# Performance work log

Measured on AMD Instinct MI355X. Metric: run time of the kernel, lower is better.

Reference implementation:

```python
import jax, jax.numpy as jnp
import numpy as np

NUM_BINS = 4
SCALE = 5.0
EPS = 1e-12

def hswish(x):
    return x * jnp.clip(x + 3.0, 0.0, 6.0) / 6.0

def l2norm(x, axis):
    n = jnp.sqrt(jnp.sum(x * x, axis=axis, keepdims=True))
    return x / jnp.maximum(n, EPS)

def setup_inputs() -> dict:
    key = jax.random.key(0)
    k0, k1, k2, k3, k4 = jax.random.split(key, 5)
    B, C, T, H, W = 8, 256, 32, 28, 28
    hidden, embd = 512, 32
    x = jax.random.normal(k0, (B, C, T, H, W), dtype=jnp.float32)
    W1 = jax.random.normal(k1, (hidden, C), dtype=jnp.float32) * (1.0 / np.sqrt(C))
    b1 = jax.random.normal(k2, (hidden,), dtype=jnp.float32) * 0.01
    W2 = jax.random.normal(k3, (embd, hidden), dtype=jnp.float32) * (1.0 / np.sqrt(hidden))
    b2 = jax.random.normal(k4, (embd,), dtype=jnp.float32) * 0.01
    return {"x": x, "W1": W1, "b1": b1, "W2": W2, "b2": b2}

def reference(x, W1, b1, W2, b2):
    B, C, T, H, W = x.shape
    # encoder: global spatial avg-pool -> 1x1x1 conv -> HSwish -> 1x1x1 conv
    pooled = jnp.mean(x, axis=(3, 4))                      # (B,C,T)
    h = hswish(jnp.einsum('hc,bct->bht', W1, pooled) + b1[None, :, None])
    embds = jnp.einsum('eh,bht->bet', W2, h) + b2[None, :, None]   # (B,E,T)
    norm_embd = l2norm(embds, axis=1)

    # --- grouping (no-grad in original) ---
    ns = jnp.sum(norm_embd[:, :, 1:] * norm_embd[:, :, :-1], axis=1)    # (B,T-1)
    # k-th smallest neighbour similarity = threshold
    smallest = -jax.lax.top_k(-ns, NUM_BINS - 1)[0]                      # ascending smallest k
    threshold = smallest[:, -1]
    edges = (ns > threshold[:, None]).astype(jnp.int32)                  # (B,T-1)
    interval_ends = jnp.concatenate(
        [jnp.zeros((B, 1), dtype=jnp.int32), 1 - edges], axis=1)        # (B,T)
    groups = jnp.cumsum(interval_ends, axis=1)                           # (B,T)
    group_ids = jnp.arange(NUM_BINS, dtype=groups.dtype)
    group_mask = (groups[:, :, None] == group_ids[None, None, :]).astype(jnp.float32)  # (B,T,K)
    group_sizes = jnp.sum(group_mask, axis=1, keepdims=True)             # (B,1,K)
    centers_sum = jnp.einsum('bet,btk->bek', norm_embd, group_mask)      # (B,E,K)
    norm_centers = l2norm(centers_sum / group_sizes, axis=1)             # (B,E,K)
    norm_centers = jax.lax.stop_gradient(norm_centers)

    similarities = jnp.einsum('bet,bek->btk', norm_embd, norm_centers)   # (B,T,K)
    weights = jax.nn.softmax(SCALE * similarities, axis=2)               # (B,T,K)
    sum_weights = jnp.sum(weights, axis=1, keepdims=True)                # (B,1,K)
    scales = jnp.where(sum_weights > 0.0, 1.0 / sum_weights, jnp.ones_like(sum_weights))
    scales = jax.lax.stop_gradient(scales)
    norm_weights = scales * weights                                      # (B,T,K)

    # weighted temporal pooling: avoids (B,C,T,K,H,W) blowup
    out = jnp.einsum('bcthw,btk->bckhw', x, norm_weights)                # (B,C,K,H,W)
    return out
```

## Files before the change

### kernel.cpp

```cpp
#include <hip/hip_runtime.h>
#include <math.h>

#define BATCH 8
#define CCH   256
#define TT    32
#define HWSZ  784
#define HID   512
#define EMB   32
#define KBINS 4
#define SCALEF 5.0f
#define EPSN  1e-12f

__global__ __launch_bounds__(512) void poolfc_kernel(
        const float* __restrict__ x,
        const float* __restrict__ W1, const float* __restrict__ b1,
        const float* __restrict__ W2, const float* __restrict__ b2,
        float* __restrict__ embds) {
    __shared__ float pc[CCH];
    __shared__ float hcol[HID];

    const int b    = blockIdx.x >> 5;
    const int t    = blockIdx.x & 31;
    const int tid  = threadIdx.x;
    const int wave = tid >> 6;
    const int lane = tid & 63;

    const float* xbt = x + (size_t)(b * CCH) * (TT * HWSZ) + (size_t)t * HWSZ;
#pragma unroll
    for (int i = 0; i < 16; ++i) {
        const int c0 = (i << 4) + wave;
        const int c1 = c0 + 8;
        const float4* xp0 = (const float4*)(xbt + (size_t)c0 * (TT * HWSZ));
        const float4* xp1 = (const float4*)(xbt + (size_t)c1 * (TT * HWSZ));
        float4 a0 = xp0[lane];
        float4 a1 = xp0[lane + 64];
        float4 a2 = xp0[lane + 128];
        float4 d0 = xp1[lane];
        float4 d1 = xp1[lane + 64];
        float4 d2 = xp1[lane + 128];
        float s0 = a0.x + a0.y + a0.z + a0.w
                 + a1.x + a1.y + a1.z + a1.w
                 + a2.x + a2.y + a2.z + a2.w;
        float s1 = d0.x + d0.y + d0.z + d0.w
                 + d1.x + d1.y + d1.z + d1.w
                 + d2.x + d2.y + d2.z + d2.w;
        if (lane < 4) {
            float4 a3 = xp0[lane + 192];
            float4 d3 = xp1[lane + 192];
            s0 += a3.x + a3.y + a3.z + a3.w;
            s1 += d3.x + d3.y + d3.z + d3.w;
        }
#pragma unroll
        for (int off = 32; off > 0; off >>= 1) {
            s0 += __shfl_down(s0, off);
            s1 += __shfl_down(s1, off);
        }
        if (lane == 0) {
            pc[c0] = s0 * (1.0f / 784.0f);
            pc[c1] = s1 * (1.0f / 784.0f);
        }
    }
    __syncthreads();

    {
        const float4* w = (const float4*)(W1 + (size_t)tid * CCH);
        const float4* p4 = (const float4*)pc;
        float acc = 0.f;
#pragma unroll 8
        for (int j = 0; j < CCH / 4; ++j) {
            float4 wv = w[j];
            float4 pv = p4[j];
            acc += wv.x * pv.x + wv.y * pv.y + wv.z * pv.z + wv.w * pv.w;
        }
        acc += b1[tid];
        float r = fminf(fmaxf(acc + 3.0f, 0.0f), 6.0f);
        hcol[tid] = acc * r * (1.0f / 6.0f);
    }
    __syncthreads();

    {
        const int e = tid >> 4;
        const int l = tid & 15;
        const float* w = W2 + (size_t)e * HID;
        float acc = 0.f;
#pragma unroll
        for (int j = 0; j < HID / 16; j++) acc += w[l + 16 * j] * hcol[l + 16 * j];
        acc += __shfl_down(acc, 8);
        acc += __shfl_down(acc, 4);
        acc += __shfl_down(acc, 2);
        acc += __shfl_down(acc, 1);
        if (l == 0) embds[((size_t)b * EMB + e) * TT + t] = acc + b2[e];
    }
}

__global__ void group_kernel(const float* __restrict__ embds, float* __restrict__ nw) {
    __shared__ float se[EMB][TT + 1];
    __shared__ float ns[TT];
    __shared__ float colinv[TT];
    __shared__ float thr_sh;
    __shared__ float cs[EMB][KBINS];
    __shared__ float wts[TT][KBINS];
    __shared__ float gsize[KBINS];
    __shared__ float kfac[KBINS];
    __shared__ int   gid[TT];

    const int b   = blockIdx.x;
    const int tid = threadIdx.x;

    for (int i = tid; i < EMB * TT; i += 256)
        se[i >> 5][i & 31] = embds[(size_t)b * EMB * TT + i];
    __syncthreads();

    if (tid < TT) {
        float s = 0.f;
        for (int e = 0; e < EMB; e++) { float v = se[e][tid]; s += v * v; }
        colinv[tid] = 1.0f / fmaxf(sqrtf(s), EPSN);
    }
    __syncthreads();
    for (int i = tid; i < EMB * TT; i += 256) {
        int e = i >> 5, t = i & 31;
        se[e][t] *= colinv[t];
    }
    __syncthreads();

    if (tid < TT - 1) {
        float s = 0.f;
        for (int e = 0; e < EMB; e++) s += se[e][tid] * se[e][tid + 1];
        ns[tid] = s;
    }
    __syncthreads();

    if (tid < TT - 1) {
        float v = ns[tid];
        int pos = 0;
        for (int j = 0; j < TT - 1; j++) {
            float u = ns[j];
            pos += (u < v) || (u == v && j < tid);
        }
        if (pos == KBINS - 2) thr_sh = v;
    }
    __syncthreads();

    if (tid < TT) {
        float thr = thr_sh;
        int g = 0;
        for (int s = 1; s <= tid; s++) g += !(ns[s - 1] > thr);
        gid[tid] = g;
    }
    __syncthreads();
    if (tid < KBINS) {
        float c = 0.f;
        for (int t = 0; t < TT; t++) c += (gid[t] == tid);
        gsize[tid] = c;
    }
    __syncthreads();

    if (tid < EMB * KBINS) {
        int e = tid >> 2, k = tid & 3;
        float s = 0.f;
        for (int t = 0; t < TT; t++) if (gid[t] == k) s += se[e][t];
        cs[e][k] = s / gsize[k];
    }
    __syncthreads();
    if (tid < KBINS) {
        float s = 0.f;
        for (int e = 0; e < EMB; e++) { float v = cs[e][tid]; s += v * v; }
        kfac[tid] = 1.0f / fmaxf(sqrtf(s), EPSN);
    }
    __syncthreads();
    if (tid < EMB * KBINS) {
        int e = tid >> 2, k = tid & 3;
        cs[e][k] *= kfac[k];
    }
    __syncthreads();

    if (tid < TT * KBINS) {
        int t = tid >> 2, k = tid & 3;
        float s = 0.f;
        for (int e = 0; e < EMB; e++) s += se[e][t] * cs[e][k];
        wts[t][k] = s * SCALEF;
    }
    __syncthreads();
    if (tid < TT) {
        float m = wts[tid][0];
        for (int k = 1; k < KBINS; k++) m = fmaxf(m, wts[tid][k]);
        float ex[KBINS]; float sum = 0.f;
        for (int k = 0; k < KBINS; k++) { ex[k] = expf(wts[tid][k] - m); sum += ex[k]; }
        float inv = 1.0f / sum;
        for (int k = 0; k < KBINS; k++) wts[tid][k] = ex[k] * inv;
    }
    __syncthreads();
    if (tid < KBINS) {
        float s = 0.f;
        for (int t = 0; t < TT; t++) s += wts[t][tid];
        kfac[tid] = (s > 0.f) ? (1.0f / s) : 1.0f;
    }
    __syncthreads();
    if (tid < TT * KBINS) {
        int t = tid >> 2, k = tid & 3;
        nw[((size_t)b * TT + t) * KBINS + k] = wts[t][k] * kfac[k];
    }
}

__global__ __launch_bounds__(128) void out_kernel(
        const float* __restrict__ x, const float* __restrict__ nw,
        float* __restrict__ out) {
    __shared__ float w[TT * KBINS];
    const int b = blockIdx.x / 392;
    const unsigned idx = (blockIdx.x % 392) * 128 + threadIdx.x;
    w[threadIdx.x] = nw[(size_t)b * TT * KBINS + threadIdx.x];
    __syncthreads();
    const unsigned c = idx / 196;
    const unsigned f = idx % 196;
    const float4* xp = (const float4*)(x + ((size_t)(b * CCH + c) * TT) * HWSZ);
    float4 acc[KBINS];
#pragma unroll
    for (int k = 0; k < KBINS; k++) { acc[k].x = 0.f; acc[k].y = 0.f; acc[k].z = 0.f; acc[k].w = 0.f; }
#pragma unroll 8
    for (int t = 0; t < TT; t++) {
        float4 v = xp[t * 196 + f];
#pragma unroll
        for (int k = 0; k < KBINS; k++) {
            float wk = w[t * KBINS + k];
            acc[k].x += v.x * wk;
            acc[k].y += v.y * wk;
            acc[k].z += v.z * wk;
            acc[k].w += v.w * wk;
        }
    }
    float4* op = (float4*)(out + ((size_t)(b * CCH + c) * KBINS) * HWSZ);
#pragma unroll
    for (int k = 0; k < KBINS; k++) op[k * 196 + f] = acc[k];
}

extern "C" void kernel_launch(void* const* d_in, const int* in_sizes, int n_in,
                              void* d_out, int out_size, void* d_ws, size_t ws_size,
                              hipStream_t stream) {
    const float* x  = (const float*)d_in[0];
    const float* W1 = (const float*)d_in[1];
    const float* b1 = (const float*)d_in[2];
    const float* W2 = (const float*)d_in[3];
    const float* b2 = (const float*)d_in[4];
    float* out = (float*)d_out;

    float* ws    = (float*)d_ws;
    float* embds = ws;
    float* nw    = embds + BATCH * EMB * TT;

    poolfc_kernel<<<BATCH * TT, 512, 0, stream>>>(x, W1, b1, W2, b2, embds);
    group_kernel<<<BATCH, 256, 0, stream>>>(embds, nw);
    out_kernel<<<BATCH * 392, 128, 0, stream>>>(x, nw, out);
}
```

Baseline: 346.1 us.

## Fuse grouping into weighted-pooling kernel, recomputing weights per block

Merges the per-batch grouping kernel into the output pooling kernel. Each of the 1568 blocks recomputes the normalized bin weights for its batch in shared memory and then does the temporal weighted sum over 256 threads, with the weights read as one float4 per timestep. This removes one kernel launch and the round trip of the weights through global memory. The cost is that the serial grouping logic (top-k, cumsum, softmax, many barriers) now runs redundantly in every block before any x loads are issued.

```diff
diff --git a/kernel.cpp b/kernel.cpp
--- a/kernel.cpp
+++ b/kernel.cpp
@@ -93,7 +93,9 @@
     }
 }
 
-__global__ void group_kernel(const float* __restrict__ embds, float* __restrict__ nw) {
+__global__ __launch_bounds__(256) void outg_kernel(
+        const float* __restrict__ x, const float* __restrict__ embds,
+        float* __restrict__ out) {
     __shared__ float se[EMB][TT + 1];
     __shared__ float ns[TT];
     __shared__ float colinv[TT];
@@ -103,8 +105,9 @@
     __shared__ float gsize[KBINS];
     __shared__ float kfac[KBINS];
     __shared__ int   gid[TT];
-
-    const int b   = blockIdx.x;
+    __shared__ float wl[TT * KBINS];
+
+    const int b   = blockIdx.x / 196;
     const int tid = threadIdx.x;
 
     for (int i = tid; i < EMB * TT; i += 256)
@@ -198,39 +201,33 @@
     __syncthreads();
     if (tid < TT * KBINS) {
         int t = tid >> 2, k = tid & 3;
-        nw[((size_t)b * TT + t) * KBINS + k] = wts[t][k] * kfac[k];
-    }
-}
-
-__global__ __launch_bounds__(128) void out_kernel(
-        const float* __restrict__ x, const float* __restrict__ nw,
-        float* __restrict__ out) {
-    __shared__ float w[TT * KBINS];
-    const int b = blockIdx.x / 392;
-    const unsigned idx = (blockIdx.x % 392) * 128 + threadIdx.x;
-    w[threadIdx.x] = nw[(size_t)b * TT * KBINS + threadIdx.x];
-    __syncthreads();
+        wl[tid] = wts[t][k] * kfac[k];
+    }
+    __syncthreads();
+
+    const unsigned idx = (blockIdx.x % 196) * 256 + tid;
     const unsigned c = idx / 196;
     const unsigned f = idx % 196;
     const float4* xp = (const float4*)(x + ((size_t)(b * CCH + c) * TT) * HWSZ);
-    float4 acc[KBINS];
-#pragma unroll
-    for (int k = 0; k < KBINS; k++) { acc[k].x = 0.f; acc[k].y = 0.f; acc[k].z = 0.f; acc[k].w = 0.f; }
+    const float4* wp = (const float4*)wl;
+    float4 a0 = {0.f, 0.f, 0.f, 0.f};
+    float4 a1 = {0.f, 0.f, 0.f, 0.f};
+    float4 a2 = {0.f, 0.f, 0.f, 0.f};
+    float4 a3 = {0.f, 0.f, 0.f, 0.f};
 #pragma unroll 8
-    for (int t = 0; t < TT; t++) {
-        float4 v = xp[t * 196 + f];
-#pragma unroll
-        for (int k = 0; k < KBINS; k++) {
-            float wk = w[t * KBINS + k];
-            acc[k].x += v.x * wk;
-            acc[k].y += v.y * wk;
-            acc[k].z += v.z * wk;
-            acc[k].w += v.w * wk;
-        }
+    for (int t = 0; t < TT; ++t) {
+        float4 v  = xp[t * 196 + f];
+        float4 wv = wp[t];
+        a0.x += v.x * wv.x; a0.y += v.y * wv.x; a0.z += v.z * wv.x; a0.w += v.w * wv.x;
+        a1.x += v.x * wv.y; a1.y += v.y * wv.y; a1.z += v.z * wv.y; a1.w += v.w * wv.y;
+        a2.x += v.x * wv.z; a2.y += v.y * wv.z; a2.z += v.z * wv.z; a2.w += v.w * wv.z;
+        a3.x += v.x * wv.w; a3.y += v.y * wv.w; a3.z += v.z * wv.w; a3.w += v.w * wv.w;
     }
     float4* op = (float4*)(out + ((size_t)(b * CCH + c) * KBINS) * HWSZ);
-#pragma unroll
-    for (int k = 0; k < KBINS; k++) op[k * 196 + f] = acc[k];
+    op[0 * 196 + f] = a0;
+    op[1 * 196 + f] = a1;
+    op[2 * 196 + f] = a2;
+    op[3 * 196 + f] = a3;
 }
 
 extern "C" void kernel_launch(void* const* d_in, const int* in_sizes, int n_in,
@@ -243,11 +240,8 @@
     const float* b2 = (const float*)d_in[4];
     float* out = (float*)d_out;
 
-    float* ws    = (float*)d_ws;
-    float* embds = ws;
-    float* nw    = embds + BATCH * EMB * TT;
+    float* embds = (float*)d_ws;
 
     poolfc_kernel<<<BATCH * TT, 512, 0, stream>>>(x, W1, b1, W2, b2, embds);
-    group_kernel<<<BATCH, 256, 0, stream>>>(embds, nw);
-    out_kernel<<<BATCH * 392, 128, 0, stream>>>(x, nw, out);
+    outg_kernel<<<BATCH * 196, 256, 0, stream>>>(x, embds, out);
 }
```

New measurement: 343.1 us. No clear change (-0.9%).
